# Kernel optimization log

Measured on AMD Instinct MI355X. Metric: run time of the kernel, lower is better.

## Reference

```python
import jax, jax.numpy as jnp
import numpy as np

B, T, N, D, H = 32, 24, 325, 64, 8
DH = D // H  # per-head dim = 8
MASK_VAL = -(2.0 ** 15) + 1.0  # -32767, as in the original


def setup_inputs() -> dict:
    key = jax.random.key(0)
    ks = jax.random.split(key, 12)
    s = 0.02
    return {
        "x": jax.random.normal(ks[0], (B, T, N, D), jnp.float32),
        "ste": jax.random.normal(ks[1], (B, T, N, D), jnp.float32),
        "Wq": jax.random.normal(ks[2], (2 * D, D), jnp.float32) * s,
        "bq": jnp.zeros((D,), jnp.float32),
        "Wk": jax.random.normal(ks[3], (2 * D, D), jnp.float32) * s,
        "bk": jnp.zeros((D,), jnp.float32),
        "Wv": jax.random.normal(ks[4], (2 * D, D), jnp.float32) * s,
        "bv": jnp.zeros((D,), jnp.float32),
        "Wo1": jax.random.normal(ks[5], (D, D), jnp.float32) * s,
        "bo1": jnp.zeros((D,), jnp.float32),
        "Wo2": jax.random.normal(ks[6], (D, D), jnp.float32) * s,
        "bo2": jnp.zeros((D,), jnp.float32),
    }


def reference(x, ste, Wq, bq, Wk, bk, Wv, bv, Wo1, bo1, Wo2, bo2):
    b, t, n, d = x.shape
    h = jnp.concatenate([x, ste], axis=-1)  # (B,T,N,2D)
    # FC layers (1x1 conv == per-position linear) with ReLU
    q = jax.nn.relu(h @ Wq + bq)  # (B,T,N,D)
    k = jax.nn.relu(h @ Wk + bk)
    v = jax.nn.relu(h @ Wv + bv)
    # split/concat head splitting == reshape last dim into (H, DH)
    q = q.reshape(b, t, n, H, DH)
    k = k.reshape(b, t, n, H, DH)
    v = v.reshape(b, t, n, H, DH)
    # attention over the time axis, independently per node and head
    attn = jnp.einsum("btnhd,bsnhd->bhnts", q, k) / jnp.sqrt(jnp.float32(DH))
    # causal mask over steps (lower-triangular), fill with -32767 as in source
    tril = jnp.tril(jnp.ones((t, t), dtype=bool))  # (T,T)
    attn = jnp.where(tril[None, None, None, :, :], attn, jnp.float32(MASK_VAL))
    p = jax.nn.softmax(attn, axis=-1)
    o = jnp.einsum("bhnts,bsnhd->btnhd", p, v).reshape(b, t, n, d)
    # output FC: D->D ReLU, then D->D linear
    out = jax.nn.relu(o @ Wo1 + bo1) @ Wo2 + bo2
    return out
```

## Files before the change

kernel.cpp:

```cpp
#include <hip/hip_runtime.h>
#include <hip/hip_bf16.h>


typedef unsigned short u16;
typedef unsigned int u32;
typedef __attribute__((ext_vector_type(8))) short bf16x8;
typedef __attribute__((ext_vector_type(4))) float f32x4;

#define B_ 32
#define T_ 24
#define N_ 325
#define D_ 64

#define WQKV_OFF 0
#define WO1_OFF  24576
#define WO2_OFF  28672
#define WS_ELS   32768

__device__ __align__(64) u16 g_ws[WS_ELS];

__device__ __forceinline__ u16 f2bf(float f) {
    u32 u = __float_as_uint(f);
    return (u16)((u + 0x7FFFu + ((u >> 16) & 1u)) >> 16);
}
__device__ __forceinline__ u32 pack2(float a, float b) {
    return (u32)f2bf(a) | ((u32)f2bf(b) << 16);
}

__global__ void ta_repack(const float* __restrict__ Wq, const float* __restrict__ Wk,
                          const float* __restrict__ Wv, const float* __restrict__ Wo1,
                          const float* __restrict__ Wo2) {
    int f = blockIdx.x * 256 + threadIdx.x;
    const float* src;
    u16* dst;
    if (f < 3072) {
        int nt = f >> 8, ks = (f >> 6) & 3, l = f & 63;
        int nn = nt * 16 + (l & 15);
        int kb = ks * 32 + ((l >> 4) & 3) * 8;
        const float* W = (nn < 64) ? Wq : (nn < 128 ? Wk : Wv);
        src = W + kb * 64 + (nn & 63);
        dst = g_ws + WQKV_OFF + f * 8;
    } else {
        int fo = f - 3072;
        int m = fo >> 9;
        int fi = fo & 511;
        int nt = fi >> 7, ks = (fi >> 6) & 1, l = fi & 63;
        int nn = nt * 16 + (l & 15);
        int kb = ks * 32 + ((l >> 4) & 3) * 8;
        src = (m ? Wo2 : Wo1) + kb * 64 + nn;
        dst = g_ws + (m ? WO2_OFF : WO1_OFF) + fi * 8;
    }
    #pragma unroll
    for (int j = 0; j < 8; ++j) dst[j] = f2bf(src[j * 64]);
}

#define SMEM_BYTES 44032

__global__ __launch_bounds__(256) void ta_mfma(
    const float* __restrict__ x,   const float* __restrict__ ste,
    const float* __restrict__ bq,  const float* __restrict__ bk,
    const float* __restrict__ bv,  const float* __restrict__ bo1,
    const float* __restrict__ bo2, float* __restrict__ out)
{
    __shared__ __align__(16) char smem[SMEM_BYTES];
    u16*   sh_h   = (u16*)smem;
    u16*   sh_o   = (u16*)(smem + 8704);
    u16*   sh_tmp = (u16*)(smem + 13312);
    float* sh_q   = (float*)(smem + 17920);
    float* sh_k   = (float*)(smem + 26624);
    float* sh_v   = (float*)(smem + 35328);

    const int tid  = threadIdx.x;
    const int w    = tid >> 6;
    const int l    = tid & 63;
    const int l15  = l & 15;
    const int quad = l >> 4;
    const int n = blockIdx.x;
    const int b = blockIdx.y;

    {
        uint4 z; z.x = z.y = z.z = z.w = 0u;
        for (int i = tid; i < SMEM_BYTES / 16; i += 256)
            *(uint4*)(smem + i * 16) = z;
    }
    __syncthreads();

    for (int i = tid; i < 384; i += 256) {
        int f = i * 8;
        int t = f >> 7, kk = f & 127;
        int gbase = ((b * T_ + t) * N_ + n) * D_;
        const float* src = (kk < 64) ? (x + gbase + kk) : (ste + gbase + kk - 64);
        float4 a = *(const float4*)src;
        float4 c = *(const float4*)(src + 4);
        uint4 o;
        o.x = pack2(a.x, a.y); o.y = pack2(a.z, a.w);
        o.z = pack2(c.x, c.y); o.w = pack2(c.z, c.w);
        *(uint4*)(sh_h + t * 136 + kk) = o;
    }
    const int col16 = w * 16 + l15;
    float bqv = bq[col16],  bkv = bk[col16],  bvv = bv[col16];
    float b1v = bo1[col16], b2v = bo2[col16];
    __syncthreads();

    bf16x8 af0_0 = *(const bf16x8*)(sh_h + l15 * 136 + 0  + quad * 8);
    bf16x8 af0_1 = *(const bf16x8*)(sh_h + l15 * 136 + 32 + quad * 8);
    bf16x8 af0_2 = *(const bf16x8*)(sh_h + l15 * 136 + 64 + quad * 8);
    bf16x8 af0_3 = *(const bf16x8*)(sh_h + l15 * 136 + 96 + quad * 8);
    bf16x8 af1_0 = *(const bf16x8*)(sh_h + (16 + l15) * 136 + 0  + quad * 8);
    bf16x8 af1_1 = *(const bf16x8*)(sh_h + (16 + l15) * 136 + 32 + quad * 8);
    bf16x8 af1_2 = *(const bf16x8*)(sh_h + (16 + l15) * 136 + 64 + quad * 8);
    bf16x8 af1_3 = *(const bf16x8*)(sh_h + (16 + l15) * 136 + 96 + quad * 8);

    {
        const int nt = w;
        f32x4 c0 = {0.f,0.f,0.f,0.f}, c1 = {0.f,0.f,0.f,0.f};
        bf16x8 bf;
        bf = *(const bf16x8*)(g_ws + WQKV_OFF + ((nt*4 + 0)*64 + l)*8);
        c0 = __builtin_amdgcn_mfma_f32_16x16x32_bf16(af0_0, bf, c0, 0,0,0);
        c1 = __builtin_amdgcn_mfma_f32_16x16x32_bf16(af1_0, bf, c1, 0,0,0);
        bf = *(const bf16x8*)(g_ws + WQKV_OFF + ((nt*4 + 1)*64 + l)*8);
        c0 = __builtin_amdgcn_mfma_f32_16x16x32_bf16(af0_1, bf, c0, 0,0,0);
        c1 = __builtin_amdgcn_mfma_f32_16x16x32_bf16(af1_1, bf, c1, 0,0,0);
        bf = *(const bf16x8*)(g_ws + WQKV_OFF + ((nt*4 + 2)*64 + l)*8);
        c0 = __builtin_amdgcn_mfma_f32_16x16x32_bf16(af0_2, bf, c0, 0,0,0);
        c1 = __builtin_amdgcn_mfma_f32_16x16x32_bf16(af1_2, bf, c1, 0,0,0);
        bf = *(const bf16x8*)(g_ws + WQKV_OFF + ((nt*4 + 3)*64 + l)*8);
        c0 = __builtin_amdgcn_mfma_f32_16x16x32_bf16(af0_3, bf, c0, 0,0,0);
        c1 = __builtin_amdgcn_mfma_f32_16x16x32_bf16(af1_3, bf, c1, 0,0,0);
        #pragma unroll
        for (int r = 0; r < 4; ++r) {
            int row0 = quad * 4 + r;
            sh_q[row0 * 68 + col16]        = fmaxf(c0[r] + bqv, 0.f);
            sh_q[(16 + row0) * 68 + col16] = fmaxf(c1[r] + bqv, 0.f);
        }
    }
    {
        const int nt = w + 4;
        f32x4 c0 = {0.f,0.f,0.f,0.f}, c1 = {0.f,0.f,0.f,0.f};
        bf16x8 bf;
        bf = *(const bf16x8*)(g_ws + WQKV_OFF + ((nt*4 + 0)*64 + l)*8);
        c0 = __builtin_amdgcn_mfma_f32_16x16x32_bf16(af0_0, bf, c0, 0,0,0);
        c1 = __builtin_amdgcn_mfma_f32_16x16x32_bf16(af1_0, bf, c1, 0,0,0);
        bf = *(const bf16x8*)(g_ws + WQKV_OFF + ((nt*4 + 1)*64 + l)*8);
        c0 = __builtin_amdgcn_mfma_f32_16x16x32_bf16(af0_1, bf, c0, 0,0,0);
        c1 = __builtin_amdgcn_mfma_f32_16x16x32_bf16(af1_1, bf, c1, 0,0,0);
        bf = *(const bf16x8*)(g_ws + WQKV_OFF + ((nt*4 + 2)*64 + l)*8);
        c0 = __builtin_amdgcn_mfma_f32_16x16x32_bf16(af0_2, bf, c0, 0,0,0);
        c1 = __builtin_amdgcn_mfma_f32_16x16x32_bf16(af1_2, bf, c1, 0,0,0);
        bf = *(const bf16x8*)(g_ws + WQKV_OFF + ((nt*4 + 3)*64 + l)*8);
        c0 = __builtin_amdgcn_mfma_f32_16x16x32_bf16(af0_3, bf, c0, 0,0,0);
        c1 = __builtin_amdgcn_mfma_f32_16x16x32_bf16(af1_3, bf, c1, 0,0,0);
        #pragma unroll
        for (int r = 0; r < 4; ++r) {
            int row0 = quad * 4 + r;
            sh_k[row0 * 68 + col16]        = fmaxf(c0[r] + bkv, 0.f);
            sh_k[(16 + row0) * 68 + col16] = fmaxf(c1[r] + bkv, 0.f);
        }
    }
    {
        const int nt = w + 8;
        f32x4 c0 = {0.f,0.f,0.f,0.f}, c1 = {0.f,0.f,0.f,0.f};
        bf16x8 bf;
        bf = *(const bf16x8*)(g_ws + WQKV_OFF + ((nt*4 + 0)*64 + l)*8);
        c0 = __builtin_amdgcn_mfma_f32_16x16x32_bf16(af0_0, bf, c0, 0,0,0);
        c1 = __builtin_amdgcn_mfma_f32_16x16x32_bf16(af1_0, bf, c1, 0,0,0);
        bf = *(const bf16x8*)(g_ws + WQKV_OFF + ((nt*4 + 1)*64 + l)*8);
        c0 = __builtin_amdgcn_mfma_f32_16x16x32_bf16(af0_1, bf, c0, 0,0,0);
        c1 = __builtin_amdgcn_mfma_f32_16x16x32_bf16(af1_1, bf, c1, 0,0,0);
        bf = *(const bf16x8*)(g_ws + WQKV_OFF + ((nt*4 + 2)*64 + l)*8);
        c0 = __builtin_amdgcn_mfma_f32_16x16x32_bf16(af0_2, bf, c0, 0,0,0);
        c1 = __builtin_amdgcn_mfma_f32_16x16x32_bf16(af1_2, bf, c1, 0,0,0);
        bf = *(const bf16x8*)(g_ws + WQKV_OFF + ((nt*4 + 3)*64 + l)*8);
        c0 = __builtin_amdgcn_mfma_f32_16x16x32_bf16(af0_3, bf, c0, 0,0,0);
        c1 = __builtin_amdgcn_mfma_f32_16x16x32_bf16(af1_3, bf, c1, 0,0,0);
        #pragma unroll
        for (int r = 0; r < 4; ++r) {
            int row0 = quad * 4 + r;
            sh_v[row0 * 68 + col16]        = fmaxf(c0[r] + bvv, 0.f);
            sh_v[(16 + row0) * 68 + col16] = fmaxf(c1[r] + bvv, 0.f);
        }
    }
    __syncthreads();

    bf16x8 w1f0 = *(const bf16x8*)(g_ws + WO1_OFF + ((w*2 + 0)*64 + l)*8);
    bf16x8 w1f1 = *(const bf16x8*)(g_ws + WO1_OFF + ((w*2 + 1)*64 + l)*8);
    bf16x8 w2f0 = *(const bf16x8*)(g_ws + WO2_OFF + ((w*2 + 0)*64 + l)*8);
    bf16x8 w2f1 = *(const bf16x8*)(g_ws + WO2_OFF + ((w*2 + 1)*64 + l)*8);
    {
        const int hi = tid >> 5;
        const int t  = tid & 31;
        if (t < 24) {
            const float* qp = sh_q + t * 68 + hi * 8;
            float qr[8];
            #pragma unroll
            for (int d = 0; d < 8; ++d) qr[d] = qp[d];
            float e[24], mx = -3.0e38f;
            #pragma unroll
            for (int s = 0; s < T_; ++s) {
                const float* kp = sh_k + s * 68 + hi * 8;
                float4 ka = *(const float4*)kp;
                float4 kb2 = *(const float4*)(kp + 4);
                float dot = qr[0] * ka.x;
                dot = fmaf(qr[1], ka.y, dot);  dot = fmaf(qr[2], ka.z, dot);
                dot = fmaf(qr[3], ka.w, dot);  dot = fmaf(qr[4], kb2.x, dot);
                dot = fmaf(qr[5], kb2.y, dot); dot = fmaf(qr[6], kb2.z, dot);
                dot = fmaf(qr[7], kb2.w, dot);
                float lg = (s <= t) ? dot * 0.35355339059327373f : -32767.0f;
                e[s] = lg;
                mx = fmaxf(mx, lg);
            }
            float sum = 0.f;
            #pragma unroll
            for (int s = 0; s < T_; ++s) { float ee = __expf(e[s] - mx); e[s] = ee; sum += ee; }
            float inv = 1.0f / sum;
            float ov[8];
            #pragma unroll
            for (int d = 0; d < 8; ++d) ov[d] = 0.f;
            #pragma unroll
            for (int s = 0; s < T_; ++s) {
                float p = e[s] * inv;
                const float* vp = sh_v + s * 68 + hi * 8;
                float4 va = *(const float4*)vp;
                float4 vb = *(const float4*)(vp + 4);
                ov[0] = fmaf(p, va.x, ov[0]); ov[1] = fmaf(p, va.y, ov[1]);
                ov[2] = fmaf(p, va.z, ov[2]); ov[3] = fmaf(p, va.w, ov[3]);
                ov[4] = fmaf(p, vb.x, ov[4]); ov[5] = fmaf(p, vb.y, ov[5]);
                ov[6] = fmaf(p, vb.z, ov[6]); ov[7] = fmaf(p, vb.w, ov[7]);
            }
            u16* op = sh_o + t * 72 + hi * 8;
            *(u32*)(op + 0) = pack2(ov[0], ov[1]);
            *(u32*)(op + 2) = pack2(ov[2], ov[3]);
            *(u32*)(op + 4) = pack2(ov[4], ov[5]);
            *(u32*)(op + 6) = pack2(ov[6], ov[7]);
        }
    }
    __syncthreads();

    {
        bf16x8 a00 = *(const bf16x8*)(sh_o + l15 * 72 + 0  + quad * 8);
        bf16x8 a01 = *(const bf16x8*)(sh_o + l15 * 72 + 32 + quad * 8);
        bf16x8 a10 = *(const bf16x8*)(sh_o + (16 + l15) * 72 + 0  + quad * 8);
        bf16x8 a11 = *(const bf16x8*)(sh_o + (16 + l15) * 72 + 32 + quad * 8);
        f32x4 c0 = {0.f,0.f,0.f,0.f}, c1 = {0.f,0.f,0.f,0.f};
        c0 = __builtin_amdgcn_mfma_f32_16x16x32_bf16(a00, w1f0, c0, 0,0,0);
        c1 = __builtin_amdgcn_mfma_f32_16x16x32_bf16(a10, w1f0, c1, 0,0,0);
        c0 = __builtin_amdgcn_mfma_f32_16x16x32_bf16(a01, w1f1, c0, 0,0,0);
        c1 = __builtin_amdgcn_mfma_f32_16x16x32_bf16(a11, w1f1, c1, 0,0,0);
        #pragma unroll
        for (int r = 0; r < 4; ++r) {
            int row0 = quad * 4 + r;
            sh_tmp[row0 * 72 + col16]        = f2bf(fmaxf(c0[r] + b1v, 0.f));
            sh_tmp[(16 + row0) * 72 + col16] = f2bf(fmaxf(c1[r] + b1v, 0.f));
        }
    }
    __syncthreads();

    {
        bf16x8 a00 = *(const bf16x8*)(sh_tmp + l15 * 72 + 0  + quad * 8);
        bf16x8 a01 = *(const bf16x8*)(sh_tmp + l15 * 72 + 32 + quad * 8);
        bf16x8 a10 = *(const bf16x8*)(sh_tmp + (16 + l15) * 72 + 0  + quad * 8);
        bf16x8 a11 = *(const bf16x8*)(sh_tmp + (16 + l15) * 72 + 32 + quad * 8);
        f32x4 c0 = {0.f,0.f,0.f,0.f}, c1 = {0.f,0.f,0.f,0.f};
        c0 = __builtin_amdgcn_mfma_f32_16x16x32_bf16(a00, w2f0, c0, 0,0,0);
        c1 = __builtin_amdgcn_mfma_f32_16x16x32_bf16(a10, w2f0, c1, 0,0,0);
        c0 = __builtin_amdgcn_mfma_f32_16x16x32_bf16(a01, w2f1, c0, 0,0,0);
        c1 = __builtin_amdgcn_mfma_f32_16x16x32_bf16(a11, w2f1, c1, 0,0,0);
        #pragma unroll
        for (int r = 0; r < 4; ++r) {
            int row0 = quad * 4 + r;
            out[((b * T_ + row0) * N_ + n) * D_ + col16] = c0[r] + b2v;
            int row1 = 16 + row0;
            if (row1 < T_)
                out[((b * T_ + row1) * N_ + n) * D_ + col16] = c1[r] + b2v;
        }
    }
}

extern "C" void kernel_launch(void* const* d_in, const int* in_sizes, int n_in,
                              void* d_out, int out_size, void* d_ws, size_t ws_size,
                              hipStream_t stream) {
    (void)in_sizes; (void)n_in; (void)out_size; (void)d_ws; (void)ws_size;
    const float* x   = (const float*)d_in[0];
    const float* ste = (const float*)d_in[1];
    const float* Wq  = (const float*)d_in[2];
    const float* bq  = (const float*)d_in[3];
    const float* Wk  = (const float*)d_in[4];
    const float* bk  = (const float*)d_in[5];
    const float* Wv  = (const float*)d_in[6];
    const float* bv  = (const float*)d_in[7];
    const float* Wo1 = (const float*)d_in[8];
    const float* bo1 = (const float*)d_in[9];
    const float* Wo2 = (const float*)d_in[10];
    const float* bo2 = (const float*)d_in[11];

    ta_repack<<<dim3(16), dim3(256), 0, stream>>>(Wq, Wk, Wv, Wo1, Wo2);
    ta_mfma<<<dim3(N_, B_), dim3(256), 0, stream>>>(
        x, ste, bq, bk, bv, bo1, bo2, (float*)d_out);
}
```

Baseline: 249.8 us.

## Shrink shared memory footprint and drop zero-fill to raise block occupancy

Reduces shared memory from about 44 KB to about 29.5 KB by aliasing the tmp buffer over the input staging buffer and packing the q/k/v buffers more tightly. It also removes the initial zero-fill pass and its barrier, and skips stores for padded rows 24-31. A launch-bounds hint of 5 blocks is added to let more blocks reside per CU. Because the buffers now alias, an extra barrier is needed before writing tmp, and the softmax scale is folded into q. The risks are the extra barrier and the padded rows of sh_o being left uninitialised, which the padded MFMA rows then read.

```diff
diff --git a/kernel.cpp b/kernel.cpp
--- a/kernel.cpp
+++ b/kernel.cpp
@@ -54,9 +54,9 @@
     for (int j = 0; j < 8; ++j) dst[j] = f2bf(src[j * 64]);
 }
 
-#define SMEM_BYTES 44032
-
-__global__ __launch_bounds__(256) void ta_mfma(
+#define SMEM_BYTES 29568
+
+__global__ __launch_bounds__(256, 5) void ta_mfma(
     const float* __restrict__ x,   const float* __restrict__ ste,
     const float* __restrict__ bq,  const float* __restrict__ bk,
     const float* __restrict__ bv,  const float* __restrict__ bo1,
@@ -64,11 +64,11 @@
 {
     __shared__ __align__(16) char smem[SMEM_BYTES];
     u16*   sh_h   = (u16*)smem;
-    u16*   sh_o   = (u16*)(smem + 8704);
-    u16*   sh_tmp = (u16*)(smem + 13312);
-    float* sh_q   = (float*)(smem + 17920);
-    float* sh_k   = (float*)(smem + 26624);
-    float* sh_v   = (float*)(smem + 35328);
+    u16*   sh_tmp = (u16*)smem;
+    u16*   sh_o   = (u16*)(smem + 6528);
+    float* sh_q   = (float*)(smem + 9984);
+    float* sh_k   = (float*)(smem + 16512);
+    float* sh_v   = (float*)(smem + 23040);
 
     const int tid  = threadIdx.x;
     const int w    = tid >> 6;
@@ -77,13 +77,6 @@
     const int quad = l >> 4;
     const int n = blockIdx.x;
     const int b = blockIdx.y;
-
-    {
-        uint4 z; z.x = z.y = z.z = z.w = 0u;
-        for (int i = tid; i < SMEM_BYTES / 16; i += 256)
-            *(uint4*)(smem + i * 16) = z;
-    }
-    __syncthreads();
 
     for (int i = tid; i < 384; i += 256) {
         int f = i * 8;
@@ -130,8 +123,14 @@
         #pragma unroll
         for (int r = 0; r < 4; ++r) {
             int row0 = quad * 4 + r;
-            sh_q[row0 * 68 + col16]        = fmaxf(c0[r] + bqv, 0.f);
-            sh_q[(16 + row0) * 68 + col16] = fmaxf(c1[r] + bqv, 0.f);
+            sh_q[row0 * 68 + col16] = fmaxf(c0[r] + bqv, 0.f);
+        }
+        if (quad < 2) {
+            #pragma unroll
+            for (int r = 0; r < 4; ++r) {
+                int row1 = 16 + quad * 4 + r;
+                sh_q[row1 * 68 + col16] = fmaxf(c1[r] + bqv, 0.f);
+            }
         }
     }
     {
@@ -153,8 +152,14 @@
         #pragma unroll
         for (int r = 0; r < 4; ++r) {
             int row0 = quad * 4 + r;
-            sh_k[row0 * 68 + col16]        = fmaxf(c0[r] + bkv, 0.f);
-            sh_k[(16 + row0) * 68 + col16] = fmaxf(c1[r] + bkv, 0.f);
+            sh_k[row0 * 68 + col16] = fmaxf(c0[r] + bkv, 0.f);
+        }
+        if (quad < 2) {
+            #pragma unroll
+            for (int r = 0; r < 4; ++r) {
+                int row1 = 16 + quad * 4 + r;
+                sh_k[row1 * 68 + col16] = fmaxf(c1[r] + bkv, 0.f);
+            }
         }
     }
     {
@@ -176,8 +181,14 @@
         #pragma unroll
         for (int r = 0; r < 4; ++r) {
             int row0 = quad * 4 + r;
-            sh_v[row0 * 68 + col16]        = fmaxf(c0[r] + bvv, 0.f);
-            sh_v[(16 + row0) * 68 + col16] = fmaxf(c1[r] + bvv, 0.f);
+            sh_v[row0 * 68 + col16] = fmaxf(c0[r] + bvv, 0.f);
+        }
+        if (quad < 2) {
+            #pragma unroll
+            for (int r = 0; r < 4; ++r) {
+                int row1 = 16 + quad * 4 + r;
+                sh_v[row1 * 68 + col16] = fmaxf(c1[r] + bvv, 0.f);
+            }
         }
     }
     __syncthreads();
@@ -193,7 +204,7 @@
             const float* qp = sh_q + t * 68 + hi * 8;
             float qr[8];
             #pragma unroll
-            for (int d = 0; d < 8; ++d) qr[d] = qp[d];
+            for (int d = 0; d < 8; ++d) qr[d] = qp[d] * 0.35355339059327373f;
             float e[24], mx = -3.0e38f;
             #pragma unroll
             for (int s = 0; s < T_; ++s) {
@@ -205,7 +216,7 @@
                 dot = fmaf(qr[3], ka.w, dot);  dot = fmaf(qr[4], kb2.x, dot);
                 dot = fmaf(qr[5], kb2.y, dot); dot = fmaf(qr[6], kb2.z, dot);
                 dot = fmaf(qr[7], kb2.w, dot);
-                float lg = (s <= t) ? dot * 0.35355339059327373f : -32767.0f;
+                float lg = (s <= t) ? dot : -32767.0f;
                 e[s] = lg;
                 mx = fmaxf(mx, lg);
             }
@@ -246,11 +257,18 @@
         c1 = __builtin_amdgcn_mfma_f32_16x16x32_bf16(a10, w1f0, c1, 0,0,0);
         c0 = __builtin_amdgcn_mfma_f32_16x16x32_bf16(a01, w1f1, c0, 0,0,0);
         c1 = __builtin_amdgcn_mfma_f32_16x16x32_bf16(a11, w1f1, c1, 0,0,0);
-        #pragma unroll
-        for (int r = 0; r < 4; ++r) {
-            int row0 = quad * 4 + r;
-            sh_tmp[row0 * 72 + col16]        = f2bf(fmaxf(c0[r] + b1v, 0.f));
-            sh_tmp[(16 + row0) * 72 + col16] = f2bf(fmaxf(c1[r] + b1v, 0.f));
+        __syncthreads();
+        #pragma unroll
+        for (int r = 0; r < 4; ++r) {
+            int row0 = quad * 4 + r;
+            sh_tmp[row0 * 72 + col16] = f2bf(fmaxf(c0[r] + b1v, 0.f));
+        }
+        if (quad < 2) {
+            #pragma unroll
+            for (int r = 0; r < 4; ++r) {
+                int row1 = 16 + quad * 4 + r;
+                sh_tmp[row1 * 72 + col16] = f2bf(fmaxf(c1[r] + b1v, 0.f));
+            }
         }
     }
     __syncthreads();
```

New measurement: 253.5 us. About the same (+1.5%).
